# Kernel tuning notes

Hardware: AMD Instinct MI355X
Metric: run time of the kernel (lower is better)

The kernel has to match this reference:

```python
import jax, jax.numpy as jnp
import numpy as np

R, M, A = 512, 256, 256
B, L = 64, 4096


def setup_inputs() -> dict:
    key = jax.random.key(0)
    k1, k2, k3, k4, k5 = jax.random.split(key, 5)
    return {
        "hidden_state": jax.random.normal(k1, (B, R), dtype=jnp.float32),
        "feature_vectors": jax.random.normal(k2, (B, L, M), dtype=jnp.float32),
        "Wa": jax.random.normal(k3, (A, R), dtype=jnp.float32) / np.sqrt(R),
        "Ua": jax.random.normal(k4, (A, M), dtype=jnp.float32) / np.sqrt(M),
        "w": jax.random.normal(k5, (A, 1), dtype=jnp.float32),
        "ba": jnp.zeros((1, A), dtype=jnp.float32),
    }


def reference(hidden_state, feature_vectors, Wa, Ua, w, ba):
    # q: [B, A] broadcast over L; k: [B, L, A]
    q = hidden_state @ Wa.T + ba                      # [B, A]
    k = jnp.einsum("blm,am->bla", feature_vectors, Ua)  # [B, L, A]
    e = jnp.tanh(q[:, None, :] + k) @ w               # [B, L, 1]
    attn = jax.nn.softmax(e, axis=1)                  # softmax over L
    context = jnp.sum(attn * feature_vectors, axis=1)  # [B, M]
    return context
```

## Files before the change

### kernel.cpp

```cpp
#include <hip/hip_runtime.h>
#include <hip/hip_bf16.h>

#define B_  64
#define R_  512
#define M_  256
#define A_  256
#define L_  4096
#define NT_ 32
#define TR_ 128

typedef float    f32x4 __attribute__((ext_vector_type(4)));
typedef _Float16 f16x8 __attribute__((ext_vector_type(8)));

__global__ __launch_bounds__(256) void k_prep(const float* __restrict__ Ua,
                                              _Float16* __restrict__ Ua16) {
  int idx = (blockIdx.x * 256 + threadIdx.x) * 4;
  f32x4 v = *(const f32x4*)(Ua + idx);
  Ua16[idx + 0] = (_Float16)v.x;
  Ua16[idx + 1] = (_Float16)v.y;
  Ua16[idx + 2] = (_Float16)v.z;
  Ua16[idx + 3] = (_Float16)v.w;
}

__global__ __launch_bounds__(256) void k_q(const float* __restrict__ h,
                                           const float* __restrict__ Wa,
                                           const float* __restrict__ ba,
                                           float* __restrict__ q) {
  int b = blockIdx.x;
  int tid = threadIdx.x;
  int wv = tid >> 6, lane = tid & 63;
  const f32x4* hp = (const f32x4*)(h + (size_t)b * R_ + lane * 8);
  f32x4 h0 = hp[0], h1 = hp[1];
#pragma unroll 4
  for (int i = 0; i < 64; ++i) {
    int a = wv * 64 + i;
    const f32x4* wp = (const f32x4*)(Wa + (size_t)a * R_ + lane * 8);
    f32x4 w0 = wp[0], w1 = wp[1];
    f32x4 pr = h0 * w0 + h1 * w1;
    float p = (pr.x + pr.y) + (pr.z + pr.w);
#pragma unroll
    for (int m = 1; m < 64; m <<= 1) p += __shfl_xor(p, m);
    if (lane == 0) q[b * A_ + a] = p + ba[a];
  }
}

__global__ __launch_bounds__(256) void k_main(const float* __restrict__ fv,
                                              const _Float16* __restrict__ Ua16,
                                              const float* __restrict__ q,
                                              const float* __restrict__ w,
                                              float* __restrict__ blkmax,
                                              float* __restrict__ blksum,
                                              float* __restrict__ blkacc) {
  __shared__ float sq[A_];
  __shared__ float sw[A_];
  __shared__ float sE[TR_];
  __shared__ float sRed[8];
  __shared__ float sAcc[4][M_];
  int tid = threadIdx.x;
  int b  = blockIdx.x >> 5;
  int l0 = (blockIdx.x & 31) * TR_;
  int wv = tid >> 6, lane = tid & 63;
  int quad = lane >> 4, l16 = lane & 15;

  sq[tid] = q[b * A_ + tid];
  sw[tid] = w[tid];

  f16x8 afrag[2][8];
#pragma unroll
  for (int rs = 0; rs < 2; ++rs) {
    const float* rowp = fv + ((size_t)b * L_ + (size_t)(l0 + wv * 32 + rs * 16 + l16)) * M_ + quad * 8;
#pragma unroll
    for (int s = 0; s < 8; ++s) {
      f32x4 x = *(const f32x4*)(rowp + s * 32);
      f32x4 y = *(const f32x4*)(rowp + s * 32 + 4);
      f16x8 f;
      f[0] = (_Float16)x.x; f[1] = (_Float16)x.y; f[2] = (_Float16)x.z; f[3] = (_Float16)x.w;
      f[4] = (_Float16)y.x; f[5] = (_Float16)y.y; f[6] = (_Float16)y.z; f[7] = (_Float16)y.w;
      afrag[rs][s] = f;
    }
  }
  __syncthreads();

  float eacc[2][4] = {{0.f, 0.f, 0.f, 0.f}, {0.f, 0.f, 0.f, 0.f}};

#pragma unroll 4
  for (int t = 0; t < 16; ++t) {
    f32x4 acc0 = 0.f, acc1 = 0.f;
    const f16x8* bp = (const f16x8*)(Ua16 + ((size_t)(t * 16 + l16) << 8) + quad * 8);
#pragma unroll
    for (int s = 0; s < 8; ++s) {
      f16x8 bf = bp[s * 4];
      acc0 = __builtin_amdgcn_mfma_f32_16x16x32_f16(afrag[0][s], bf, acc0, 0, 0, 0);
      acc1 = __builtin_amdgcn_mfma_f32_16x16x32_f16(afrag[1][s], bf, acc1, 0, 0, 0);
    }
    float qc = sq[t * 16 + l16], wc = sw[t * 16 + l16];
#pragma unroll
    for (int i = 0; i < 4; ++i) {
      float x0 = qc + acc0[i];
      float e0 = __expf(2.0f * x0);
      eacc[0][i] += (1.0f - 2.0f * __builtin_amdgcn_rcpf(e0 + 1.0f)) * wc;
      float x1 = qc + acc1[i];
      float e1 = __expf(2.0f * x1);
      eacc[1][i] += (1.0f - 2.0f * __builtin_amdgcn_rcpf(e1 + 1.0f)) * wc;
    }
  }

#pragma unroll
  for (int rs = 0; rs < 2; ++rs)
#pragma unroll
    for (int i = 0; i < 4; ++i) {
      float v = eacc[rs][i];
      v += __shfl_xor(v, 1); v += __shfl_xor(v, 2);
      v += __shfl_xor(v, 4); v += __shfl_xor(v, 8);
      if (l16 == 0) sE[wv * 32 + rs * 16 + quad * 4 + i] = v;
    }
  __syncthreads();

  float m = (tid < TR_) ? sE[tid] : -1e30f;
#pragma unroll
  for (int k = 1; k < 64; k <<= 1) m = fmaxf(m, __shfl_xor(m, k));
  if (lane == 0) sRed[wv] = m;
  __syncthreads();
  float mx = fmaxf(fmaxf(sRed[0], sRed[1]), fmaxf(sRed[2], sRed[3]));

  float p0 = __expf(sE[wv * 32 + l16] - mx);
  float p1 = __expf(sE[wv * 32 + 16 + l16] - mx);

  float ps = (quad == 0) ? (p0 + p1) : 0.f;
#pragma unroll
  for (int k = 1; k < 64; k <<= 1) ps += __shfl_xor(ps, k);
  if (lane == 0) sRed[4 + wv] = ps;

#pragma unroll
  for (int s = 0; s < 8; ++s) {
    float c[8];
#pragma unroll
    for (int j = 0; j < 8; ++j)
      c[j] = p0 * (float)afrag[0][s][j] + p1 * (float)afrag[1][s][j];
#pragma unroll
    for (int k = 1; k < 16; k <<= 1) {
#pragma unroll
      for (int j = 0; j < 8; ++j) c[j] += __shfl_xor(c[j], k);
    }
    if (l16 == 0) {
#pragma unroll
      for (int j = 0; j < 8; ++j) sAcc[wv][s * 32 + quad * 8 + j] = c[j];
    }
  }
  __syncthreads();

  float colsum = (sAcc[0][tid] + sAcc[1][tid]) + (sAcc[2][tid] + sAcc[3][tid]);
  blkacc[(size_t)blockIdx.x * M_ + tid] = colsum;
  if (tid == 0) {
    blkmax[blockIdx.x] = mx;
    blksum[blockIdx.x] = (sRed[4] + sRed[5]) + (sRed[6] + sRed[7]);
  }
}

__global__ __launch_bounds__(256) void k_fin(const float* __restrict__ blkmax,
                                             const float* __restrict__ blksum,
                                             const float* __restrict__ blkacc,
                                             float* __restrict__ out) {
  __shared__ float sSc[NT_];
  int b = blockIdx.x, t = threadIdx.x;
  float M = -1e30f;
#pragma unroll
  for (int i = 0; i < NT_; ++i) M = fmaxf(M, blkmax[b * NT_ + i]);
  if (t < NT_) sSc[t] = __expf(blkmax[b * NT_ + t] - M);
  __syncthreads();
  float acc = 0.f, S = 0.f;
#pragma unroll 4
  for (int i = 0; i < NT_; ++i) {
    float sc = sSc[i];
    S += blksum[b * NT_ + i] * sc;
    acc += blkacc[(size_t)(b * NT_ + i) * M_ + t] * sc;
  }
  out[b * M_ + t] = acc / S;
}

extern "C" void kernel_launch(void* const* d_in, const int* in_sizes, int n_in,
                              void* d_out, int out_size, void* d_ws, size_t ws_size,
                              hipStream_t stream) {
  const float* h  = (const float*)d_in[0];
  const float* fv = (const float*)d_in[1];
  const float* Wa = (const float*)d_in[2];
  const float* Ua = (const float*)d_in[3];
  const float* w  = (const float*)d_in[4];
  const float* ba = (const float*)d_in[5];
  float* out = (float*)d_out;

  char* ws = (char*)d_ws;
  float*    q      = (float*)(ws);
  _Float16* Ua16   = (_Float16*)(ws + 65536);
  float*    blkmax = (float*)(ws + 196608);
  float*    blksum = (float*)(ws + 204800);
  float*    blkacc = (float*)(ws + 212992);

  k_prep<<<dim3(64), dim3(256), 0, stream>>>(Ua, Ua16);
  k_q<<<dim3(B_), dim3(256), 0, stream>>>(h, Wa, ba, q);
  k_main<<<dim3(B_ * NT_), dim3(256), 0, stream>>>(fv, Ua16, q, w, blkmax, blksum, blkacc);
  k_fin<<<dim3(B_), dim3(256), 0, stream>>>(blkmax, blksum, blkacc, out);
}
```

Baseline: 555.5 us.

## Double rows per block, stage features through LDS, pre-swizzle Ua fragments

Each block now covers 256 sequence rows instead of 128, so every wave holds four MFMA row fragments and reuses each loaded Ua fragment across four MFMAs instead of two. Feature rows are loaded with fully coalesced row-contiguous float4 reads, converted to fp16, and rearranged into MFMA fragment order through a per-wave LDS scratch buffer. Ua is pre-swizzled in the prep kernel so the B-fragment loads become contiguous. The costs are doubled register pressure for the A fragments (occupancy hint of 2 blocks), extra LDS traffic, and half as many blocks, which reduces parallelism and latency hiding.

Measured after the change: 466.1 us. -16.1%, faster.

```diff
diff --git a/kernel.cpp b/kernel.cpp
--- a/kernel.cpp
+++ b/kernel.cpp
@@ -6,20 +6,26 @@
 #define M_  256
 #define A_  256
 #define L_  4096
-#define NT_ 32
-#define TR_ 128
-
-typedef float    f32x4 __attribute__((ext_vector_type(4)));
-typedef _Float16 f16x8 __attribute__((ext_vector_type(8)));
+#define TR_ 256
+#define NT2_ (L_ / TR_)
+
+typedef float    f32x4  __attribute__((ext_vector_type(4)));
+typedef _Float16 f16x8  __attribute__((ext_vector_type(8)));
+typedef _Float16 f16x4  __attribute__((ext_vector_type(4)));
 
 __global__ __launch_bounds__(256) void k_prep(const float* __restrict__ Ua,
-                                              _Float16* __restrict__ Ua16) {
-  int idx = (blockIdx.x * 256 + threadIdx.x) * 4;
-  f32x4 v = *(const f32x4*)(Ua + idx);
-  Ua16[idx + 0] = (_Float16)v.x;
-  Ua16[idx + 1] = (_Float16)v.y;
-  Ua16[idx + 2] = (_Float16)v.z;
-  Ua16[idx + 3] = (_Float16)v.w;
+                                              _Float16* __restrict__ UaSw) {
+  int gid = blockIdx.x * 256 + threadIdx.x;
+  int a  = gid >> 6;
+  int m0 = (gid & 63) * 4;
+  f32x4 v = *(const f32x4*)(Ua + (size_t)a * M_ + m0);
+  int t = a >> 4, l16 = a & 15;
+  int s = m0 >> 5, quad = (m0 >> 3) & 3, j = m0 & 7;
+  size_t idx = ((size_t)((t * 8 + s) * 64 + l16 * 4 + quad)) * 8 + j;
+  f16x4 h;
+  h[0] = (_Float16)v.x; h[1] = (_Float16)v.y;
+  h[2] = (_Float16)v.z; h[3] = (_Float16)v.w;
+  *(f16x4*)(UaSw + idx) = h;
 }
 
 __global__ __launch_bounds__(256) void k_q(const float* __restrict__ h,
@@ -44,107 +50,121 @@
   }
 }
 
-__global__ __launch_bounds__(256) void k_main(const float* __restrict__ fv,
-                                              const _Float16* __restrict__ Ua16,
-                                              const float* __restrict__ q,
-                                              const float* __restrict__ w,
-                                              float* __restrict__ blkmax,
-                                              float* __restrict__ blksum,
-                                              float* __restrict__ blkacc) {
+__global__ __launch_bounds__(256, 2) void k_main(const float* __restrict__ fv,
+                                                 const _Float16* __restrict__ UaSw,
+                                                 const float* __restrict__ q,
+                                                 const float* __restrict__ w,
+                                                 float* __restrict__ blkmax,
+                                                 float* __restrict__ blksum,
+                                                 float* __restrict__ blkacc) {
+  __shared__ __align__(16) _Float16 sA[4][4096];
   __shared__ float sq[A_];
   __shared__ float sw[A_];
   __shared__ float sE[TR_];
   __shared__ float sRed[8];
   __shared__ float sAcc[4][M_];
   int tid = threadIdx.x;
-  int b  = blockIdx.x >> 5;
-  int l0 = (blockIdx.x & 31) * TR_;
+  int b  = blockIdx.x >> 4;
+  int l0 = (blockIdx.x & 15) * TR_;
   int wv = tid >> 6, lane = tid & 63;
   int quad = lane >> 4, l16 = lane & 15;
 
   sq[tid] = q[b * A_ + tid];
   sw[tid] = w[tid];
 
-  f16x8 afrag[2][8];
-#pragma unroll
-  for (int rs = 0; rs < 2; ++rs) {
-    const float* rowp = fv + ((size_t)b * L_ + (size_t)(l0 + wv * 32 + rs * 16 + l16)) * M_ + quad * 8;
+  int s_w  = lane >> 3;
+  int qd_w = (lane >> 1) & 3;
+  int jh_w = (lane & 1) * 4;
+  _Float16* wbase = &sA[wv][0];
+
+  f16x8 afrag[4][8];
+#pragma unroll
+  for (int c = 0; c < 4; ++c) {
+    const float* rowp = fv + ((size_t)b * L_ + (size_t)(l0 + wv * 64 + c * 16)) * M_ + lane * 4;
+#pragma unroll
+    for (int i = 0; i < 16; ++i) {
+      f32x4 v = *(const f32x4*)(rowp + (size_t)i * M_);
+      f16x4 h;
+      h[0] = (_Float16)v.x; h[1] = (_Float16)v.y;
+      h[2] = (_Float16)v.z; h[3] = (_Float16)v.w;
+      *(f16x4*)(wbase + s_w * 512 + (i * 4 + qd_w) * 8 + jh_w) = h;
+    }
+#pragma unroll
+    for (int s = 0; s < 8; ++s)
+      afrag[c][s] = *(const f16x8*)(wbase + s * 512 + (l16 * 4 + quad) * 8);
+  }
+  __syncthreads();
+
+  float eacc[4][4] = {{0,0,0,0},{0,0,0,0},{0,0,0,0},{0,0,0,0}};
+
+#pragma unroll 2
+  for (int t = 0; t < 16; ++t) {
+    f32x4 acc0 = 0.f, acc1 = 0.f, acc2 = 0.f, acc3 = 0.f;
+    const f16x8* bp = (const f16x8*)(UaSw + ((size_t)(t * 8) * 64 + (l16 * 4 + quad)) * 8);
 #pragma unroll
     for (int s = 0; s < 8; ++s) {
-      f32x4 x = *(const f32x4*)(rowp + s * 32);
-      f32x4 y = *(const f32x4*)(rowp + s * 32 + 4);
-      f16x8 f;
-      f[0] = (_Float16)x.x; f[1] = (_Float16)x.y; f[2] = (_Float16)x.z; f[3] = (_Float16)x.w;
-      f[4] = (_Float16)y.x; f[5] = (_Float16)y.y; f[6] = (_Float16)y.z; f[7] = (_Float16)y.w;
-      afrag[rs][s] = f;
-    }
-  }
-  __syncthreads();
-
-  float eacc[2][4] = {{0.f, 0.f, 0.f, 0.f}, {0.f, 0.f, 0.f, 0.f}};
-
-#pragma unroll 4
-  for (int t = 0; t < 16; ++t) {
-    f32x4 acc0 = 0.f, acc1 = 0.f;
-    const f16x8* bp = (const f16x8*)(Ua16 + ((size_t)(t * 16 + l16) << 8) + quad * 8);
-#pragma unroll
-    for (int s = 0; s < 8; ++s) {
-      f16x8 bf = bp[s * 4];
+      f16x8 bf = bp[s * 64];
       acc0 = __builtin_amdgcn_mfma_f32_16x16x32_f16(afrag[0][s], bf, acc0, 0, 0, 0);
       acc1 = __builtin_amdgcn_mfma_f32_16x16x32_f16(afrag[1][s], bf, acc1, 0, 0, 0);
+      acc2 = __builtin_amdgcn_mfma_f32_16x16x32_f16(afrag[2][s], bf, acc2, 0, 0, 0);
+      acc3 = __builtin_amdgcn_mfma_f32_16x16x32_f16(afrag[3][s], bf, acc3, 0, 0, 0);
     }
     float qc = sq[t * 16 + l16], wc = sw[t * 16 + l16];
 #pragma unroll
     for (int i = 0; i < 4; ++i) {
       float x0 = qc + acc0[i];
-      float e0 = __expf(2.0f * x0);
-      eacc[0][i] += (1.0f - 2.0f * __builtin_amdgcn_rcpf(e0 + 1.0f)) * wc;
+      eacc[0][i] += (1.0f - 2.0f * __builtin_amdgcn_rcpf(__expf(2.0f * x0) + 1.0f)) * wc;
       float x1 = qc + acc1[i];
-      float e1 = __expf(2.0f * x1);
-      eacc[1][i] += (1.0f - 2.0f * __builtin_amdgcn_rcpf(e1 + 1.0f)) * wc;
-    }
-  }
-
-#pragma unroll
-  for (int rs = 0; rs < 2; ++rs)
+      eacc[1][i] += (1.0f - 2.0f * __builtin_amdgcn_rcpf(__expf(2.0f * x1) + 1.0f)) * wc;
+      float x2 = qc + acc2[i];
+      eacc[2][i] += (1.0f - 2.0f * __builtin_amdgcn_rcpf(__expf(2.0f * x2) + 1.0f)) * wc;
+      float x3 = qc + acc3[i];
+      eacc[3][i] += (1.0f - 2.0f * __builtin_amdgcn_rcpf(__expf(2.0f * x3) + 1.0f)) * wc;
+    }
+  }
+
+#pragma unroll
+  for (int c = 0; c < 4; ++c)
 #pragma unroll
     for (int i = 0; i < 4; ++i) {
-      float v = eacc[rs][i];
+      float v = eacc[c][i];
       v += __shfl_xor(v, 1); v += __shfl_xor(v, 2);
       v += __shfl_xor(v, 4); v += __shfl_xor(v, 8);
-      if (l16 == 0) sE[wv * 32 + rs * 16 + quad * 4 + i] = v;
-    }
-  __syncthreads();
-
-  float m = (tid < TR_) ? sE[tid] : -1e30f;
+      if (l16 == 0) sE[wv * 64 + c * 16 + quad * 4 + i] = v;
+    }
+  __syncthreads();
+
+  float m = sE[tid];
 #pragma unroll
   for (int k = 1; k < 64; k <<= 1) m = fmaxf(m, __shfl_xor(m, k));
   if (lane == 0) sRed[wv] = m;
   __syncthreads();
   float mx = fmaxf(fmaxf(sRed[0], sRed[1]), fmaxf(sRed[2], sRed[3]));
 
-  float p0 = __expf(sE[wv * 32 + l16] - mx);
-  float p1 = __expf(sE[wv * 32 + 16 + l16] - mx);
-
-  float ps = (quad == 0) ? (p0 + p1) : 0.f;
+  float p[4];
+#pragma unroll
+  for (int c = 0; c < 4; ++c) p[c] = __expf(sE[wv * 64 + c * 16 + l16] - mx);
+
+  float ps = (quad == 0) ? ((p[0] + p[1]) + (p[2] + p[3])) : 0.f;
 #pragma unroll
   for (int k = 1; k < 64; k <<= 1) ps += __shfl_xor(ps, k);
   if (lane == 0) sRed[4 + wv] = ps;
 
 #pragma unroll
   for (int s = 0; s < 8; ++s) {
-    float c[8];
+    float cj[8];
 #pragma unroll
     for (int j = 0; j < 8; ++j)
-      c[j] = p0 * (float)afrag[0][s][j] + p1 * (float)afrag[1][s][j];
+      cj[j] = p[0] * (float)afrag[0][s][j] + p[1] * (float)afrag[1][s][j] +
+              p[2] * (float)afrag[2][s][j] + p[3] * (float)afrag[3][s][j];
 #pragma unroll
     for (int k = 1; k < 16; k <<= 1) {
 #pragma unroll
-      for (int j = 0; j < 8; ++j) c[j] += __shfl_xor(c[j], k);
+      for (int j = 0; j < 8; ++j) cj[j] += __shfl_xor(cj[j], k);
     }
     if (l16 == 0) {
 #pragma unroll
-      for (int j = 0; j < 8; ++j) sAcc[wv][s * 32 + quad * 8 + j] = c[j];
+      for (int j = 0; j < 8; ++j) sAcc[wv][s * 32 + quad * 8 + j] = cj[j];
     }
   }
   __syncthreads();
@@ -161,19 +181,19 @@
                                              const float* __restrict__ blksum,
                                              const float* __restrict__ blkacc,
                                              float* __restrict__ out) {
-  __shared__ float sSc[NT_];
+  __shared__ float sSc[NT2_];
   int b = blockIdx.x, t = threadIdx.x;
   float M = -1e30f;
 #pragma unroll
-  for (int i = 0; i < NT_; ++i) M = fmaxf(M, blkmax[b * NT_ + i]);
-  if (t < NT_) sSc[t] = __expf(blkmax[b * NT_ + t] - M);
+  for (int i = 0; i < NT2_; ++i) M = fmaxf(M, blkmax[b * NT2_ + i]);
+  if (t < NT2_) sSc[t] = __expf(blkmax[b * NT2_ + t] - M);
   __syncthreads();
   float acc = 0.f, S = 0.f;
 #pragma unroll 4
-  for (int i = 0; i < NT_; ++i) {
+  for (int i = 0; i < NT2_; ++i) {
     float sc = sSc[i];
-    S += blksum[b * NT_ + i] * sc;
-    acc += blkacc[(size_t)(b * NT_ + i) * M_ + t] * sc;
+    S += blksum[b * NT2_ + i] * sc;
+    acc += blkacc[(size_t)(b * NT2_ + i) * M_ + t] * sc;
   }
   out[b * M_ + t] = acc / S;
 }
@@ -191,13 +211,13 @@
 
   char* ws = (char*)d_ws;
   float*    q      = (float*)(ws);
-  _Float16* Ua16   = (_Float16*)(ws + 65536);
+  _Float16* UaSw   = (_Float16*)(ws + 65536);
   float*    blkmax = (float*)(ws + 196608);
-  float*    blksum = (float*)(ws + 204800);
-  float*    blkacc = (float*)(ws + 212992);
-
-  k_prep<<<dim3(64), dim3(256), 0, stream>>>(Ua, Ua16);
+  float*    blksum = (float*)(ws + 200704);
+  float*    blkacc = (float*)(ws + 204800);
+
+  k_prep<<<dim3(64), dim3(256), 0, stream>>>(Ua, UaSw);
   k_q<<<dim3(B_), dim3(256), 0, stream>>>(h, Wa, ba, q);
-  k_main<<<dim3(B_ * NT_), dim3(256), 0, stream>>>(fv, Ua16, q, w, blkmax, blksum, blkacc);
+  k_main<<<dim3(B_ * NT2_), dim3(256), 0, stream>>>(fv, UaSw, q, w, blkmax, blksum, blkacc);
   k_fin<<<dim3(B_), dim3(256), 0, stream>>>(blkmax, blksum, blkacc, out);
 }
```
